# Kernel optimization log

Hardware: AMD Instinct MI355X
Metric: run time of the kernel (lower is better)

## Reference

```python
import jax, jax.numpy as jnp
import numpy as np

B, D, DK, DV, NH = 4, 256, 32, 32, 8
HS, WS, RATIO = 64, 64, 2
NQ = HS * WS
EPS_LN = 1e-5
EPS_IN = 1e-5


def setup_inputs() -> dict:
    key = jax.random.key(0)
    ks = jax.random.split(key, 16)
    f = jax.random.normal
    inp = {
        'query': f(ks[0], (B, NQ, D), jnp.float32),
        'key':   f(ks[1], (B, NQ, D), jnp.float32),
        'value': f(ks[2], (B, NQ, D), jnp.float32),
        # Linear weights stored (in, out); torch init std=0.001, bias 0 -- use small std for stability
        'Wq': f(ks[3], (D, DK * NH), jnp.float32) * 0.02,
        'bq': jnp.zeros((DK * NH,), jnp.float32),
        'Wk': f(ks[4], (D, DK * NH), jnp.float32) * 0.02,
        'bk': jnp.zeros((DK * NH,), jnp.float32),
        'Wv': f(ks[5], (D, DV * NH), jnp.float32) * 0.02,
        'bv': jnp.zeros((DV * NH,), jnp.float32),
        'Wo': f(ks[6], (NH * DV, D), jnp.float32) * 0.02,
        'bo': jnp.zeros((D,), jnp.float32),
        # sr_conv: Conv2d(D, D, k=ratio+1=3, stride=2, pad=1), OIHW
        'sr_w': f(ks[7], (D, D, 3, 3), jnp.float32) * (1.0 / np.sqrt(9 * D)),
        'sr_b': jnp.zeros((D,), jnp.float32),
        'ln_g': jnp.ones((D,), jnp.float32),
        'ln_b': jnp.zeros((D,), jnp.float32),
        # transform conv: Conv2d(h, h, 1) -> store as (h, h)
        'tf_w': f(ks[8], (NH, NH), jnp.float32) * (1.0 / np.sqrt(NH)),
        'tf_b': jnp.zeros((NH,), jnp.float32),
    }
    return inp


def _layernorm(x, g, b):
    mu = jnp.mean(x, axis=-1, keepdims=True)
    var = jnp.var(x, axis=-1, keepdims=True)
    return (x - mu) * jax.lax.rsqrt(var + EPS_LN) * g + b


def reference(query, key, value, Wq, bq, Wk, bk, Wv, bv, Wo, bo,
              sr_w, sr_b, ln_g, ln_b, tf_w, tf_b):
    b_s = query.shape[0]
    # q: (b, h, nq, dk)
    q = (query @ Wq + bq).reshape(b_s, NQ, NH, DK).transpose(0, 2, 1, 3)
    # spatial reduction of query: (b, c, H, W) -> conv stride 2 -> (b, c, H/2, W/2)
    x = query.transpose(0, 2, 1).reshape(b_s, D, HS, WS)
    x = jax.lax.conv_general_dilated(
        x, sr_w, window_strides=(RATIO, RATIO), padding=[(1, 1), (1, 1)],
        dimension_numbers=('NCHW', 'OIHW', 'NCHW')) + sr_b[None, :, None, None]
    nk = x.shape[2] * x.shape[3]
    x = x.reshape(b_s, D, nk).transpose(0, 2, 1)  # (b, nk, c)
    x = _layernorm(x, ln_g, ln_b)
    k = (x @ Wk + bk).reshape(b_s, nk, NH, DK).transpose(0, 2, 3, 1)  # (b,h,dk,nk)
    v = (x @ Wv + bv).reshape(b_s, nk, NH, DV).transpose(0, 2, 1, 3)  # (b,h,nk,dv)
    # scores (b,h,nq,nk)
    att = jnp.einsum('bhqd,bhdk->bhqk', q, k) / np.float32(np.sqrt(DK))
    # transform: 1x1 conv mixing heads, softmax over keys, InstanceNorm2d(h) (no affine)
    att = jnp.einsum('oi,biqk->boqk', tf_w, att) + tf_b[None, :, None, None]
    att = jax.nn.softmax(att, axis=-1)
    mu = jnp.mean(att, axis=(2, 3), keepdims=True)
    var = jnp.var(att, axis=(2, 3), keepdims=True)
    att = (att - mu) * jax.lax.rsqrt(var + EPS_IN)
    out = jnp.einsum('bhqk,bhkd->bhqd', att, v)  # (b,h,nq,dv)
    out = out.transpose(0, 2, 1, 3).reshape(b_s, NQ, NH * DV)
    return out @ Wo + bo
```

## Files before the change

kernel.cpp:

```cpp
#include <hip/hip_runtime.h>
#include <hip/hip_bf16.h>
#include <cstdint>


typedef _Float16 f16;
typedef f16 f16x4 __attribute__((ext_vector_type(4)));
typedef f16 f16x8 __attribute__((ext_vector_type(8)));
typedef float f32x4 __attribute__((ext_vector_type(4)));

__global__ void zero32_kernel(float* __restrict__ p){ p[threadIdx.x] = 0.f; }

__launch_bounds__(256)
__global__ void qcvt_kernel(const float* __restrict__ in, f16* __restrict__ out){
    size_t idx = ((size_t)blockIdx.x*256 + threadIdx.x) * 8;
    float4 a = *(const float4*)&in[idx];
    float4 b = *(const float4*)&in[idx+4];
    f16x8 h = { (f16)a.x,(f16)a.y,(f16)a.z,(f16)a.w,(f16)b.x,(f16)b.y,(f16)b.z,(f16)b.w };
    *(f16x8*)&out[idx] = h;
}

__launch_bounds__(256)
__global__ void wcvtT_kernel(const float* __restrict__ W, f16* __restrict__ WT){
    __shared__ float L[32][33];
    int r0 = blockIdx.x*32, c0 = blockIdx.y*32;
    int t = threadIdx.x;
    int rr = t >> 3, cc0 = (t & 7)*4;
    float4 v = *(const float4*)&W[(size_t)(r0+rr)*256 + c0 + cc0];
    L[rr][cc0] = v.x; L[rr][cc0+1] = v.y; L[rr][cc0+2] = v.z; L[rr][cc0+3] = v.w;
    __syncthreads();
    int c = t >> 3, rg = (t & 7)*4;
    f16x4 h = { (f16)L[rg][c], (f16)L[rg+1][c], (f16)L[rg+2][c], (f16)L[rg+3][c] };
    *(f16x4*)&WT[(size_t)(c0+c)*256 + r0 + rg] = h;
}

__launch_bounds__(256)
__global__ void convwT_kernel(const float* __restrict__ w, f16* __restrict__ wtT){
    int o = blockIdx.x, t = threadIdx.x;
    #pragma unroll
    for (int kk = 0; kk < 9; ++kk)
        wtT[(size_t)o*2304 + kk*256 + t] = (f16)w[(size_t)o*2304 + t*9 + kk];
}

template<int BM, int BN, bool OUTF16>
__launch_bounds__(256)
__global__ void mfma_gemm(const f16* __restrict__ A, const f16* __restrict__ BT,
                          const float* __restrict__ bias, void* __restrict__ Cout, int K){
    constexpr int MI = BM/32, NI = BN/32;
    __shared__ f16 As[BM][40];
    __shared__ f16 Bs[BN][40];
    int t = threadIdx.x;
    int wid = t >> 6, l = t & 63;
    int wr = wid >> 1, wc = wid & 1;
    int lr = l & 15, lg = l >> 4;
    int m0 = blockIdx.x * BM, n0 = blockIdx.y * BN;

    f32x4 acc[MI][NI] = {};
    for (int k0 = 0; k0 < K; k0 += 32){
        #pragma unroll
        for (int i = 0; i < BM/64; ++i){
            int e = t + i*256, r = e >> 2, c8 = (e & 3)*8;
            *(f16x8*)&As[r][c8] = *(const f16x8*)&A[(size_t)(m0+r)*K + k0 + c8];
        }
        #pragma unroll
        for (int i = 0; i < BN/64; ++i){
            int e = t + i*256, r = e >> 2, c8 = (e & 3)*8;
            *(f16x8*)&Bs[r][c8] = *(const f16x8*)&BT[(size_t)(n0+r)*K + k0 + c8];
        }
        __syncthreads();
        f16x8 af[MI], bf[NI];
        #pragma unroll
        for (int mi = 0; mi < MI; ++mi)
            af[mi] = *(const f16x8*)&As[wr*(BM/2) + mi*16 + lr][lg*8];
        #pragma unroll
        for (int ni = 0; ni < NI; ++ni)
            bf[ni] = *(const f16x8*)&Bs[wc*(BN/2) + ni*16 + lr][lg*8];
        #pragma unroll
        for (int mi = 0; mi < MI; ++mi)
            #pragma unroll
            for (int ni = 0; ni < NI; ++ni)
                acc[mi][ni] = __builtin_amdgcn_mfma_f32_16x16x32_f16(af[mi], bf[ni], acc[mi][ni], 0, 0, 0);
        __syncthreads();
    }
    #pragma unroll
    for (int mi = 0; mi < MI; ++mi){
        #pragma unroll
        for (int ni = 0; ni < NI; ++ni){
            int n = n0 + wc*(BN/2) + ni*16 + lr;
            float bv = bias[n];
            #pragma unroll
            for (int j = 0; j < 4; ++j){
                int m = m0 + wr*(BM/2) + mi*16 + lg*4 + j;
                float v = acc[mi][ni][j] + bv;
                if (OUTF16) ((f16*)Cout)[(size_t)m*256 + n] = (f16)v;
                else        ((float*)Cout)[(size_t)m*256 + n] = v;
            }
        }
    }
}

__launch_bounds__(256)
__global__ void conv_mfma_kernel(const f16* __restrict__ qh, const f16* __restrict__ wtT,
                                 const float* __restrict__ srb, float* __restrict__ Xc){
    __shared__ f16 As[64][40];
    __shared__ f16 Bs[64][40];
    int t = threadIdx.x;
    int wid = t >> 6, l = t & 63;
    int wr = wid >> 1, wc = wid & 1;
    int lr = l & 15, lg = l >> 4;
    int m0 = blockIdx.x * 64, n0 = blockIdx.y * 64;

    int r = t >> 2, c8 = (t & 3)*8;
    int m = m0 + r;
    int bb = m >> 10, pos = m & 1023;
    int oh = pos >> 5, ow = pos & 31;
    const f16* qb = qh + (size_t)bb*4096*256;

    f32x4 acc[2][2] = {};
    for (int k0 = 0; k0 < 2304; k0 += 32){
        int khkw = k0 >> 8;
        int kh = (khkw < 3) ? 0 : ((khkw < 6) ? 1 : 2);
        int kw = khkw - kh*3;
        int ih = oh*2 - 1 + kh, iw = ow*2 - 1 + kw;
        int kc = (k0 & 255) + c8;
        f16x8 av = {};
        if ((unsigned)ih < 64u && (unsigned)iw < 64u)
            av = *(const f16x8*)&qb[((size_t)(ih*64 + iw))*256 + kc];
        *(f16x8*)&As[r][c8] = av;
        *(f16x8*)&Bs[r][c8] = *(const f16x8*)&wtT[(size_t)(n0+r)*2304 + k0 + c8];
        __syncthreads();
        f16x8 af[2], bf[2];
        #pragma unroll
        for (int mi = 0; mi < 2; ++mi)
            af[mi] = *(const f16x8*)&As[wr*32 + mi*16 + lr][lg*8];
        #pragma unroll
        for (int ni = 0; ni < 2; ++ni)
            bf[ni] = *(const f16x8*)&Bs[wc*32 + ni*16 + lr][lg*8];
        #pragma unroll
        for (int mi = 0; mi < 2; ++mi)
            #pragma unroll
            for (int ni = 0; ni < 2; ++ni)
                acc[mi][ni] = __builtin_amdgcn_mfma_f32_16x16x32_f16(af[mi], bf[ni], acc[mi][ni], 0, 0, 0);
        __syncthreads();
    }
    #pragma unroll
    for (int mi = 0; mi < 2; ++mi){
        #pragma unroll
        for (int ni = 0; ni < 2; ++ni){
            int n = n0 + wc*32 + ni*16 + lr;
            float bv = srb[n];
            #pragma unroll
            for (int j = 0; j < 4; ++j){
                int mm = m0 + wr*32 + mi*16 + lg*4 + j;
                Xc[(size_t)mm*256 + n] = acc[mi][ni][j] + bv;
            }
        }
    }
}

__launch_bounds__(256)
__global__ void ln_kernel(const float* __restrict__ X, f16* __restrict__ Xo,
                          const float* __restrict__ g, const float* __restrict__ b){
    __shared__ float red[256];
    int row = blockIdx.x, t = threadIdx.x;
    float v = X[(size_t)row*256 + t];
    red[t] = v; __syncthreads();
    #pragma unroll
    for (int s=128; s>0; s>>=1){
        if (t < s) red[t] += red[t+s];
        __syncthreads();
    }
    float mu = red[0] * (1.f/256.f);
    __syncthreads();
    float dv = v - mu;
    red[t] = dv*dv; __syncthreads();
    #pragma unroll
    for (int s=128; s>0; s>>=1){
        if (t < s) red[t] += red[t+s];
        __syncthreads();
    }
    float var = red[0] * (1.f/256.f);
    Xo[(size_t)row*256 + t] = (f16)(dv * rsqrtf(var + 1e-5f) * g[t] + b[t]);
}

__launch_bounds__(256)
__global__ void vtran_kernel(const float* __restrict__ V, f16* __restrict__ VT){
    __shared__ float LT[32][33];
    int b = blockIdx.z, k0 = blockIdx.x*32, d0 = blockIdx.y*32;
    int t = threadIdx.x;
    int k = t >> 3, c0 = (t & 7)*4;
    float4 v = *(const float4*)&V[((size_t)(b*1024 + k0 + k))*256 + d0 + c0];
    LT[k][c0] = v.x; LT[k][c0+1] = v.y; LT[k][c0+2] = v.z; LT[k][c0+3] = v.w;
    __syncthreads();
    int d = t >> 3, kc0 = (t & 7)*4;
    f16x4 h = { (f16)LT[kc0][d], (f16)LT[kc0+1][d], (f16)LT[kc0+2][d], (f16)LT[kc0+3][d] };
    *(f16x4*)&VT[((size_t)(b*256 + d0 + d))*1024 + k0 + kc0] = h;
}

__launch_bounds__(256)
__global__ void colsum2_kernel(const f16* __restrict__ VT, float* __restrict__ csum){
    __shared__ float red[256];
    int bd = blockIdx.x, t = threadIdx.x;
    f16x4 h = *(const f16x4*)&VT[(size_t)bd*1024 + t*4];
    red[t] = (float)h[0] + (float)h[1] + (float)h[2] + (float)h[3];
    __syncthreads();
    #pragma unroll
    for (int s = 128; s > 0; s >>= 1){
        if (t < s) red[t] += red[t+s];
        __syncthreads();
    }
    if (t == 0) csum[bd] = red[0];
}

__launch_bounds__(512, 4)
__global__ void attn2_kernel(const f16* __restrict__ Qph, const f16* __restrict__ Kh,
                             const f16* __restrict__ VTh, const float* __restrict__ tfw,
                             const float* __restrict__ tfb, const float* __restrict__ csum,
                             float* __restrict__ outu, float* __restrict__ ssq){
    __shared__ f16 QL[32][264];
    __shared__ f16 KL[32][264];
    __shared__ f16 VTL[256][40];

    const int t  = threadIdx.x;
    const int bb = blockIdx.x >> 7;
    const int q0 = (blockIdx.x & 127) * 32;
    const int o  = t >> 6;
    const int l  = t & 63;
    const int g  = l >> 4;
    const int r  = l & 15;

    #pragma unroll
    for (int it = 0; it < 2; ++it){
        int e = t + it*512;
        int row = e >> 5, c0 = (e & 31)*8;
        *(f16x8*)&QL[row][c0] = *(const f16x8*)&Qph[((size_t)(bb*4096 + q0 + row))*256 + c0];
    }
    __syncthreads();

    const float tb = tfb[o];
    f16x8 qf[2][8];
    #pragma unroll
    for (int i = 0; i < 8; ++i){
        f16 sc = (f16)(tfw[o*8 + i] * 0.17677669529663687f);
        f16x8 scv = { sc,sc,sc,sc,sc,sc,sc,sc };
        #pragma unroll
        for (int qs = 0; qs < 2; ++qs){
            f16x8 v = *(const f16x8*)&QL[qs*16 + r][i*32 + g*8];
            qf[qs][i] = v * scv;
        }
    }

    f32x4 oacc[2][2] = { { {0,0,0,0},{0,0,0,0} }, { {0,0,0,0},{0,0,0,0} } };
    float s_part[2]  = {0.f, 0.f};
    float q2_part[2] = {0.f, 0.f};

    const f16* Khb = Kh  + (size_t)bb*1024*256;
    const f16* Vtb = VTh + (size_t)bb*256*1024;

    for (int kc = 0; kc < 1024; kc += 32){
        #pragma unroll
        for (int it = 0; it < 2; ++it){
            int e = t + it*512;
            int row = e >> 5, c = (e & 31)*8;
            *(f16x8*)&KL[row][c] = *(const f16x8*)&Khb[(size_t)(kc + row)*256 + c];
            int d = e >> 2, qt = (e & 3)*8;
            *(f16x8*)&VTL[d][qt] = *(const f16x8*)&Vtb[(size_t)d*1024 + kc + qt];
        }
        __syncthreads();
        #pragma unroll
        for (int ks = 0; ks < 2; ++ks){
            f16x8 kf[8];
            #pragma unroll
            for (int i = 0; i < 8; ++i)
                kf[i] = *(const f16x8*)&KL[ks*16 + r][i*32 + g*8];
            f16x4 va[2];
            #pragma unroll
            for (int dh = 0; dh < 2; ++dh)
                va[dh] = *(const f16x4*)&VTL[o*32 + dh*16 + r][ks*16 + g*4];
            #pragma unroll
            for (int qs = 0; qs < 2; ++qs){
                f32x4 acc = {0,0,0,0};
                #pragma unroll
                for (int i = 0; i < 8; ++i)
                    acc = __builtin_amdgcn_mfma_f32_16x16x32_f16(kf[i], qf[qs][i], acc, 0, 0, 0);
                f16x4 pb;
                float ps = 0.f, ps2 = 0.f;
                #pragma unroll
                for (int j = 0; j < 4; ++j){
                    float p = __expf(acc[j] + tb);
                    ps += p; ps2 += p*p;
                    pb[j] = (f16)(p - 1.0f);
                }
                s_part[qs]  += ps;
                q2_part[qs] += ps2;
                #pragma unroll
                for (int dh = 0; dh < 2; ++dh)
                    oacc[qs][dh] = __builtin_amdgcn_mfma_f32_16x16x16f16(va[dh], pb, oacc[qs][dh], 0, 0, 0);
            }
        }
        __syncthreads();
    }

    float s2tot = 0.f;
    #pragma unroll
    for (int qs = 0; qs < 2; ++qs){
        float s = s_part[qs];
        s += __shfl_xor(s, 16);
        s += __shfl_xor(s, 32);
        float inv = 1.0f / s;
        float corrf = (1.0f - s * (1.0f/1024.0f)) * inv;
        float q2 = q2_part[qs];
        q2 += __shfl_xor(q2, 16);
        q2 += __shfl_xor(q2, 32);
        s2tot += q2 * inv * inv;
        int q = q0 + qs*16 + r;
        #pragma unroll
        for (int dh = 0; dh < 2; ++dh){
            int d = o*32 + dh*16 + g*4;
            float4 cs = *(const float4*)&csum[bb*256 + d];
            float4 ov;
            ov.x = oacc[qs][dh][0]*inv + cs.x*corrf;
            ov.y = oacc[qs][dh][1]*inv + cs.y*corrf;
            ov.z = oacc[qs][dh][2]*inv + cs.z*corrf;
            ov.w = oacc[qs][dh][3]*inv + cs.w*corrf;
            *(float4*)&outu[((size_t)(bb*4096 + q))*256 + d] = ov;
        }
    }
    s2tot *= 0.25f;
    #pragma unroll
    for (int off = 1; off < 64; off <<= 1)
        s2tot += __shfl_xor(s2tot, off);
    if (l == 0) atomicAdd(&ssq[bb*8 + o], s2tot);
}

__global__ void rs_kernel(const float* __restrict__ ssq, float* __restrict__ rs){
    int t = threadIdx.x;
    const float mu = 1.f/1024.f;
    float var = ssq[t] * (1.f/(4096.f*1024.f)) - mu*mu;
    rs[t] = rsqrtf(var + 1e-5f);
}

__launch_bounds__(256)
__global__ void final_mfma_kernel(const float* __restrict__ A, const f16* __restrict__ WoT,
                                  const float* __restrict__ rsb, const float* __restrict__ bo,
                                  float* __restrict__ C){
    __shared__ f16 As[128][40];
    __shared__ f16 Bs[128][40];
    int t = threadIdx.x;
    int wid = t >> 6, l = t & 63;
    int wr = wid >> 1, wc = wid & 1;
    int lr = l & 15, lg = l >> 4;
    int m0 = blockIdx.x * 128, n0 = blockIdx.y * 128;
    int bbatch = m0 >> 12;

    f32x4 acc[4][4] = {};
    for (int k0 = 0; k0 < 256; k0 += 32){
        float rsk = rsb[bbatch*8 + (k0 >> 5)];
        #pragma unroll
        for (int i = 0; i < 2; ++i){
            int e = t + i*256, r = e >> 2, c8 = (e & 3)*8;
            const float* ap = &A[(size_t)(m0+r)*256 + k0 + c8];
            float4 v0 = *(const float4*)ap;
            float4 v1 = *(const float4*)(ap+4);
            f16x8 h = { (f16)(v0.x*rsk),(f16)(v0.y*rsk),(f16)(v0.z*rsk),(f16)(v0.w*rsk),
                        (f16)(v1.x*rsk),(f16)(v1.y*rsk),(f16)(v1.z*rsk),(f16)(v1.w*rsk) };
            *(f16x8*)&As[r][c8] = h;
        }
        #pragma unroll
        for (int i = 0; i < 2; ++i){
            int e = t + i*256, r = e >> 2, c8 = (e & 3)*8;
            *(f16x8*)&Bs[r][c8] = *(const f16x8*)&WoT[(size_t)(n0+r)*256 + k0 + c8];
        }
        __syncthreads();
        f16x8 af[4], bf[4];
        #pragma unroll
        for (int mi = 0; mi < 4; ++mi)
            af[mi] = *(const f16x8*)&As[wr*64 + mi*16 + lr][lg*8];
        #pragma unroll
        for (int ni = 0; ni < 4; ++ni)
            bf[ni] = *(const f16x8*)&Bs[wc*64 + ni*16 + lr][lg*8];
        #pragma unroll
        for (int mi = 0; mi < 4; ++mi)
            #pragma unroll
            for (int ni = 0; ni < 4; ++ni)
                acc[mi][ni] = __builtin_amdgcn_mfma_f32_16x16x32_f16(af[mi], bf[ni], acc[mi][ni], 0, 0, 0);
        __syncthreads();
    }
    #pragma unroll
    for (int mi = 0; mi < 4; ++mi){
        #pragma unroll
        for (int ni = 0; ni < 4; ++ni){
            int n = n0 + wc*64 + ni*16 + lr;
            float bv = bo[n];
            #pragma unroll
            for (int j = 0; j < 4; ++j){
                int m = m0 + wr*64 + mi*16 + lg*4 + j;
                C[(size_t)m*256 + n] = acc[mi][ni][j] + bv;
            }
        }
    }
}

extern "C" void kernel_launch(void* const* d_in, const int* in_sizes, int n_in,
                              void* d_out, int out_size, void* d_ws, size_t ws_size,
                              hipStream_t stream) {
    const float* query = (const float*)d_in[0];
    const float* Wq  = (const float*)d_in[3];
    const float* bq  = (const float*)d_in[4];
    const float* Wk  = (const float*)d_in[5];
    const float* bk  = (const float*)d_in[6];
    const float* Wv  = (const float*)d_in[7];
    const float* bv  = (const float*)d_in[8];
    const float* Wo  = (const float*)d_in[9];
    const float* bo  = (const float*)d_in[10];
    const float* srw = (const float*)d_in[11];
    const float* srb = (const float*)d_in[12];
    const float* lng = (const float*)d_in[13];
    const float* lnb = (const float*)d_in[14];
    const float* tfw = (const float*)d_in[15];
    const float* tfb = (const float*)d_in[16];
    float* out = (float*)d_out;

    float* ws = (float*)d_ws;
    float* outu  = ws;
    f16*   qh    = (f16*)(ws + 4194304);
    f16*   qbh   = (f16*)(ws + 6291456);
    float* xconv = ws + 8388608;
    float* vbuf  = ws + 9437184;
    f16*   xh    = (f16*)(ws + 10485760);
    f16*   kh    = (f16*)(ws + 11010048);
    f16*   vth   = (f16*)(ws + 11534336);
    f16*   wtT   = (f16*)(ws + 12058624);
    f16*   WqT   = (f16*)(ws + 12353536);
    f16*   WkT   = (f16*)(ws + 12386304);
    f16*   WvT   = (f16*)(ws + 12419072);
    f16*   WoT   = (f16*)(ws + 12451840);
    float* csum  = ws + 12484608;
    float* ssq   = ws + 12485632;
    float* rsb   = ws + 12485664;

    zero32_kernel<<<1, 32, 0, stream>>>(ssq);
    qcvt_kernel<<<2048, 256, 0, stream>>>(query, qh);
    wcvtT_kernel<<<dim3(8,8), 256, 0, stream>>>(Wq, WqT);
    wcvtT_kernel<<<dim3(8,8), 256, 0, stream>>>(Wk, WkT);
    wcvtT_kernel<<<dim3(8,8), 256, 0, stream>>>(Wv, WvT);
    wcvtT_kernel<<<dim3(8,8), 256, 0, stream>>>(Wo, WoT);
    convwT_kernel<<<256, 256, 0, stream>>>(srw, wtT);

    mfma_gemm<128,128,true><<<dim3(128,2), 256, 0, stream>>>(qh, WqT, bq, qbh, 256);
    conv_mfma_kernel<<<dim3(64,4), 256, 0, stream>>>(qh, wtT, srb, xconv);
    ln_kernel<<<4096, 256, 0, stream>>>(xconv, xh, lng, lnb);
    mfma_gemm<64,64,true><<<dim3(64,4), 256, 0, stream>>>(xh, WkT, bk, kh, 256);
    mfma_gemm<64,64,false><<<dim3(64,4), 256, 0, stream>>>(xh, WvT, bv, vbuf, 256);
    vtran_kernel<<<dim3(32, 8, 4), 256, 0, stream>>>(vbuf, vth);
    colsum2_kernel<<<1024, 256, 0, stream>>>(vth, csum);
    attn2_kernel<<<512, 512, 0, stream>>>(qbh, kh, vth, tfw, tfb, csum, outu, ssq);
    rs_kernel<<<1, 32, 0, stream>>>(ssq, rsb);
    final_mfma_kernel<<<dim3(128,2), 256, 0, stream>>>(outu, WoT, rsb, bo, out);
}
```

Baseline: 323.9 us.

## Double-buffer GEMM/conv/attention tiles and fuse V transpose, colsum, and zeroing

Adds register-prefetched double-buffered LDS staging to the projection GEMMs, the strided conv, the attention loop and the output GEMM, cutting one barrier per K-step and overlapping global loads with MFMA. The V projection now writes the transposed fp16 V directly and accumulates column sums with atomics, which removes the vtran and colsum kernels and the fp32 V buffer. Zeroing is folded into the query conversion, the four weight transposes are batched into one launch, and the attention softmax uses exp2 with log2e folded into the scale. This costs more shared memory per block, which may lower occupancy, and the atomic column sums make the summation order nondeterministic.

```diff
diff --git a/kernel.cpp b/kernel.cpp
--- a/kernel.cpp
+++ b/kernel.cpp
@@ -8,19 +8,28 @@
 typedef f16 f16x8 __attribute__((ext_vector_type(8)));
 typedef float f32x4 __attribute__((ext_vector_type(4)));
 
-__global__ void zero32_kernel(float* __restrict__ p){ p[threadIdx.x] = 0.f; }
-
-__launch_bounds__(256)
-__global__ void qcvt_kernel(const float* __restrict__ in, f16* __restrict__ out){
+__launch_bounds__(256)
+__global__ void qcvt_zero_kernel(const float* __restrict__ in, f16* __restrict__ out,
+                                 float* __restrict__ csum, float* __restrict__ ssq){
     size_t idx = ((size_t)blockIdx.x*256 + threadIdx.x) * 8;
     float4 a = *(const float4*)&in[idx];
     float4 b = *(const float4*)&in[idx+4];
     f16x8 h = { (f16)a.x,(f16)a.y,(f16)a.z,(f16)a.w,(f16)b.x,(f16)b.y,(f16)b.z,(f16)b.w };
     *(f16x8*)&out[idx] = h;
-}
-
-__launch_bounds__(256)
-__global__ void wcvtT_kernel(const float* __restrict__ W, f16* __restrict__ WT){
+    if (blockIdx.x == 0){
+        #pragma unroll
+        for (int i = 0; i < 4; ++i) csum[threadIdx.x + i*256] = 0.f;
+        if (threadIdx.x < 32) ssq[threadIdx.x] = 0.f;
+    }
+}
+
+__launch_bounds__(256)
+__global__ void wcvtT4_kernel(const float* __restrict__ W0, const float* __restrict__ W1,
+                              const float* __restrict__ W2, const float* __restrict__ W3,
+                              f16* __restrict__ T0, f16* __restrict__ T1,
+                              f16* __restrict__ T2, f16* __restrict__ T3){
+    const float* W = (blockIdx.z==0)?W0:(blockIdx.z==1)?W1:(blockIdx.z==2)?W2:W3;
+    f16* WT = (blockIdx.z==0)?T0:(blockIdx.z==1)?T1:(blockIdx.z==2)?T2:T3;
     __shared__ float L[32][33];
     int r0 = blockIdx.x*32, c0 = blockIdx.y*32;
     int t = threadIdx.x;
@@ -41,106 +50,161 @@
         wtT[(size_t)o*2304 + kk*256 + t] = (f16)w[(size_t)o*2304 + t*9 + kk];
 }
 
-template<int BM, int BN, bool OUTF16>
-__launch_bounds__(256)
-__global__ void mfma_gemm(const f16* __restrict__ A, const f16* __restrict__ BT,
-                          const float* __restrict__ bias, void* __restrict__ Cout, int K){
+template<int BM, int BN, int OUTMODE>
+__launch_bounds__(256)
+__global__ void mfma_gemm2(const f16* __restrict__ A, const f16* __restrict__ BT,
+                           const float* __restrict__ bias, void* __restrict__ Cout,
+                           f16* __restrict__ VT, float* __restrict__ csum, int K){
     constexpr int MI = BM/32, NI = BN/32;
-    __shared__ f16 As[BM][40];
-    __shared__ f16 Bs[BN][40];
+    constexpr int AL = BM/64, BL = BN/64;
+    __shared__ f16 As[2][BM][40];
+    __shared__ f16 Bs[2][BN][40];
     int t = threadIdx.x;
     int wid = t >> 6, l = t & 63;
     int wr = wid >> 1, wc = wid & 1;
     int lr = l & 15, lg = l >> 4;
     int m0 = blockIdx.x * BM, n0 = blockIdx.y * BN;
+    int r = t >> 2, c8 = (t & 3)*8;
+
+    f16x8 ra[AL], rb[BL];
+    auto loadc = [&](int k0){
+        #pragma unroll
+        for (int i = 0; i < AL; ++i)
+            ra[i] = *(const f16x8*)&A[(size_t)(m0 + r + i*64)*K + k0 + c8];
+        #pragma unroll
+        for (int i = 0; i < BL; ++i)
+            rb[i] = *(const f16x8*)&BT[(size_t)(n0 + r + i*64)*K + k0 + c8];
+    };
+    auto writec = [&](int b){
+        #pragma unroll
+        for (int i = 0; i < AL; ++i) *(f16x8*)&As[b][r + i*64][c8] = ra[i];
+        #pragma unroll
+        for (int i = 0; i < BL; ++i) *(f16x8*)&Bs[b][r + i*64][c8] = rb[i];
+    };
+
+    loadc(0); writec(0); loadc(32);
+    __syncthreads();
 
     f32x4 acc[MI][NI] = {};
-    for (int k0 = 0; k0 < K; k0 += 32){
-        #pragma unroll
-        for (int i = 0; i < BM/64; ++i){
-            int e = t + i*256, r = e >> 2, c8 = (e & 3)*8;
-            *(f16x8*)&As[r][c8] = *(const f16x8*)&A[(size_t)(m0+r)*K + k0 + c8];
-        }
-        #pragma unroll
-        for (int i = 0; i < BN/64; ++i){
-            int e = t + i*256, r = e >> 2, c8 = (e & 3)*8;
-            *(f16x8*)&Bs[r][c8] = *(const f16x8*)&BT[(size_t)(n0+r)*K + k0 + c8];
-        }
-        __syncthreads();
+    const int nsteps = K >> 5;
+    for (int s = 0; s < nsteps; ++s){
+        int cb = s & 1;
         f16x8 af[MI], bf[NI];
         #pragma unroll
         for (int mi = 0; mi < MI; ++mi)
-            af[mi] = *(const f16x8*)&As[wr*(BM/2) + mi*16 + lr][lg*8];
+            af[mi] = *(const f16x8*)&As[cb][wr*(BM/2) + mi*16 + lr][lg*8];
         #pragma unroll
         for (int ni = 0; ni < NI; ++ni)
-            bf[ni] = *(const f16x8*)&Bs[wc*(BN/2) + ni*16 + lr][lg*8];
+            bf[ni] = *(const f16x8*)&Bs[cb][wc*(BN/2) + ni*16 + lr][lg*8];
+        if (s + 1 < nsteps){
+            writec(cb^1);
+            if (s + 2 < nsteps) loadc((s+2)*32);
+        }
         #pragma unroll
         for (int mi = 0; mi < MI; ++mi)
             #pragma unroll
             for (int ni = 0; ni < NI; ++ni)
                 acc[mi][ni] = __builtin_amdgcn_mfma_f32_16x16x32_f16(af[mi], bf[ni], acc[mi][ni], 0, 0, 0);
-        __syncthreads();
-    }
-    #pragma unroll
-    for (int mi = 0; mi < MI; ++mi){
+        if (s + 1 < nsteps) __syncthreads();
+    }
+
+    if (OUTMODE == 1){
+        #pragma unroll
+        for (int mi = 0; mi < MI; ++mi){
+            #pragma unroll
+            for (int ni = 0; ni < NI; ++ni){
+                int n = n0 + wc*(BN/2) + ni*16 + lr;
+                float bv = bias[n];
+                #pragma unroll
+                for (int j = 0; j < 4; ++j){
+                    int m = m0 + wr*(BM/2) + mi*16 + lg*4 + j;
+                    ((f16*)Cout)[(size_t)m*256 + n] = (f16)(acc[mi][ni][j] + bv);
+                }
+            }
+        }
+    } else {
+        int b = m0 >> 10;
         #pragma unroll
         for (int ni = 0; ni < NI; ++ni){
             int n = n0 + wc*(BN/2) + ni*16 + lr;
             float bv = bias[n];
-            #pragma unroll
-            for (int j = 0; j < 4; ++j){
-                int m = m0 + wr*(BM/2) + mi*16 + lg*4 + j;
-                float v = acc[mi][ni][j] + bv;
-                if (OUTF16) ((f16*)Cout)[(size_t)m*256 + n] = (f16)v;
-                else        ((float*)Cout)[(size_t)m*256 + n] = v;
-            }
-        }
-    }
-}
-
-__launch_bounds__(256)
-__global__ void conv_mfma_kernel(const f16* __restrict__ qh, const f16* __restrict__ wtT,
-                                 const float* __restrict__ srb, float* __restrict__ Xc){
-    __shared__ f16 As[64][40];
-    __shared__ f16 Bs[64][40];
+            float csp = 0.f;
+            #pragma unroll
+            for (int mi = 0; mi < MI; ++mi){
+                f16x4 hv;
+                #pragma unroll
+                for (int j = 0; j < 4; ++j){
+                    f16 h = (f16)(acc[mi][ni][j] + bv);
+                    hv[j] = h;
+                    csp += (float)h;
+                }
+                int m = m0 + wr*(BM/2) + mi*16 + lg*4;
+                *(f16x4*)&VT[((size_t)(b*256 + n))*1024 + (m & 1023)] = hv;
+            }
+            csp += __shfl_xor(csp, 16);
+            csp += __shfl_xor(csp, 32);
+            if (lg == 0) atomicAdd(&csum[b*256 + n], csp);
+        }
+    }
+}
+
+__launch_bounds__(256)
+__global__ void conv2_kernel(const f16* __restrict__ qh, const f16* __restrict__ wtT,
+                             const float* __restrict__ srb, float* __restrict__ Xc){
+    __shared__ f16 As[2][64][40];
+    __shared__ f16 Bs[2][64][40];
     int t = threadIdx.x;
     int wid = t >> 6, l = t & 63;
     int wr = wid >> 1, wc = wid & 1;
     int lr = l & 15, lg = l >> 4;
     int m0 = blockIdx.x * 64, n0 = blockIdx.y * 64;
-
     int r = t >> 2, c8 = (t & 3)*8;
     int m = m0 + r;
-    int bb = m >> 10, pos = m & 1023;
+    int bbq = m >> 10, pos = m & 1023;
     int oh = pos >> 5, ow = pos & 31;
-    const f16* qb = qh + (size_t)bb*4096*256;
-
-    f32x4 acc[2][2] = {};
-    for (int k0 = 0; k0 < 2304; k0 += 32){
+    const f16* qb = qh + (size_t)bbq*4096*256;
+
+    f16x8 ra, rbv;
+    auto loadc = [&](int k0){
         int khkw = k0 >> 8;
         int kh = (khkw < 3) ? 0 : ((khkw < 6) ? 1 : 2);
         int kw = khkw - kh*3;
         int ih = oh*2 - 1 + kh, iw = ow*2 - 1 + kw;
         int kc = (k0 & 255) + c8;
-        f16x8 av = {};
+        f16x8 v = {};
         if ((unsigned)ih < 64u && (unsigned)iw < 64u)
-            av = *(const f16x8*)&qb[((size_t)(ih*64 + iw))*256 + kc];
-        *(f16x8*)&As[r][c8] = av;
-        *(f16x8*)&Bs[r][c8] = *(const f16x8*)&wtT[(size_t)(n0+r)*2304 + k0 + c8];
-        __syncthreads();
+            v = *(const f16x8*)&qb[((size_t)(ih*64 + iw))*256 + kc];
+        ra = v;
+        rbv = *(const f16x8*)&wtT[(size_t)(n0+r)*2304 + k0 + c8];
+    };
+    auto writec = [&](int b){
+        *(f16x8*)&As[b][r][c8] = ra;
+        *(f16x8*)&Bs[b][r][c8] = rbv;
+    };
+
+    loadc(0); writec(0); loadc(32);
+    __syncthreads();
+
+    f32x4 acc[2][2] = {};
+    for (int s = 0; s < 72; ++s){
+        int cb = s & 1;
         f16x8 af[2], bf[2];
         #pragma unroll
         for (int mi = 0; mi < 2; ++mi)
-            af[mi] = *(const f16x8*)&As[wr*32 + mi*16 + lr][lg*8];
+            af[mi] = *(const f16x8*)&As[cb][wr*32 + mi*16 + lr][lg*8];
         #pragma unroll
         for (int ni = 0; ni < 2; ++ni)
-            bf[ni] = *(const f16x8*)&Bs[wc*32 + ni*16 + lr][lg*8];
+            bf[ni] = *(const f16x8*)&Bs[cb][wc*32 + ni*16 + lr][lg*8];
+        if (s < 71){
+            writec(cb^1);
+            if (s < 70) loadc((s+2)*32);
+        }
         #pragma unroll
         for (int mi = 0; mi < 2; ++mi)
             #pragma unroll
             for (int ni = 0; ni < 2; ++ni)
                 acc[mi][ni] = __builtin_amdgcn_mfma_f32_16x16x32_f16(af[mi], bf[ni], acc[mi][ni], 0, 0, 0);
-        __syncthreads();
+        if (s < 71) __syncthreads();
     }
     #pragma unroll
     for (int mi = 0; mi < 2; ++mi){
@@ -182,43 +246,14 @@
     Xo[(size_t)row*256 + t] = (f16)(dv * rsqrtf(var + 1e-5f) * g[t] + b[t]);
 }
 
-__launch_bounds__(256)
-__global__ void vtran_kernel(const float* __restrict__ V, f16* __restrict__ VT){
-    __shared__ float LT[32][33];
-    int b = blockIdx.z, k0 = blockIdx.x*32, d0 = blockIdx.y*32;
-    int t = threadIdx.x;
-    int k = t >> 3, c0 = (t & 7)*4;
-    float4 v = *(const float4*)&V[((size_t)(b*1024 + k0 + k))*256 + d0 + c0];
-    LT[k][c0] = v.x; LT[k][c0+1] = v.y; LT[k][c0+2] = v.z; LT[k][c0+3] = v.w;
-    __syncthreads();
-    int d = t >> 3, kc0 = (t & 7)*4;
-    f16x4 h = { (f16)LT[kc0][d], (f16)LT[kc0+1][d], (f16)LT[kc0+2][d], (f16)LT[kc0+3][d] };
-    *(f16x4*)&VT[((size_t)(b*256 + d0 + d))*1024 + k0 + kc0] = h;
-}
-
-__launch_bounds__(256)
-__global__ void colsum2_kernel(const f16* __restrict__ VT, float* __restrict__ csum){
-    __shared__ float red[256];
-    int bd = blockIdx.x, t = threadIdx.x;
-    f16x4 h = *(const f16x4*)&VT[(size_t)bd*1024 + t*4];
-    red[t] = (float)h[0] + (float)h[1] + (float)h[2] + (float)h[3];
-    __syncthreads();
-    #pragma unroll
-    for (int s = 128; s > 0; s >>= 1){
-        if (t < s) red[t] += red[t+s];
-        __syncthreads();
-    }
-    if (t == 0) csum[bd] = red[0];
-}
-
 __launch_bounds__(512, 4)
-__global__ void attn2_kernel(const f16* __restrict__ Qph, const f16* __restrict__ Kh,
+__global__ void attn3_kernel(const f16* __restrict__ Qph, const f16* __restrict__ Kh,
                              const f16* __restrict__ VTh, const float* __restrict__ tfw,
                              const float* __restrict__ tfb, const float* __restrict__ csum,
                              float* __restrict__ outu, float* __restrict__ ssq){
-    __shared__ f16 QL[32][264];
-    __shared__ f16 KL[32][264];
-    __shared__ f16 VTL[256][40];
+    __shared__ f16 KL[2][32][264];
+    __shared__ f16 VTL[2][256][40];
+    f16 (*QL)[264] = KL[1];
 
     const int t  = threadIdx.x;
     const int bb = blockIdx.x >> 7;
@@ -228,19 +263,49 @@
     const int g  = l >> 4;
     const int r  = l & 15;
 
+    const f16* Khb = Kh  + (size_t)bb*1024*256;
+    const f16* Vtb = VTh + (size_t)bb*256*1024;
+
+    f16x8 rk[2], rv[2];
     #pragma unroll
     for (int it = 0; it < 2; ++it){
         int e = t + it*512;
-        int row = e >> 5, c0 = (e & 31)*8;
-        *(f16x8*)&QL[row][c0] = *(const f16x8*)&Qph[((size_t)(bb*4096 + q0 + row))*256 + c0];
-    }
-    __syncthreads();
-
-    const float tb = tfb[o];
+        int row = e >> 5, c = (e & 31)*8;
+        rk[it] = *(const f16x8*)&Khb[(size_t)row*256 + c];
+        int d = e >> 2, qt = (e & 3)*8;
+        rv[it] = *(const f16x8*)&Vtb[(size_t)d*1024 + qt];
+    }
+    #pragma unroll
+    for (int it = 0; it < 2; ++it){
+        int e = t + it*512;
+        int row = e >> 5, c = (e & 31)*8;
+        f16x8 qv = *(const f16x8*)&Qph[((size_t)(bb*4096 + q0 + row))*256 + c];
+        *(f16x8*)&QL[row][c] = qv;
+    }
+    #pragma unroll
+    for (int it = 0; it < 2; ++it){
+        int e = t + it*512;
+        int row = e >> 5, c = (e & 31)*8;
+        *(f16x8*)&KL[0][row][c] = rk[it];
+        int d = e >> 2, qt = (e & 3)*8;
+        *(f16x8*)&VTL[0][d][qt] = rv[it];
+    }
+    #pragma unroll
+    for (int it = 0; it < 2; ++it){
+        int e = t + it*512;
+        int row = e >> 5, c = (e & 31)*8;
+        rk[it] = *(const f16x8*)&Khb[(size_t)(32 + row)*256 + c];
+        int d = e >> 2, qt = (e & 3)*8;
+        rv[it] = *(const f16x8*)&Vtb[(size_t)d*1024 + 32 + qt];
+    }
+    __syncthreads();
+
+    const float LOG2E = 1.4426950408889634f;
+    const float tb2 = tfb[o] * LOG2E;
     f16x8 qf[2][8];
     #pragma unroll
     for (int i = 0; i < 8; ++i){
-        f16 sc = (f16)(tfw[o*8 + i] * 0.17677669529663687f);
+        f16 sc = (f16)(tfw[o*8 + i] * (0.17677669529663687f * LOG2E));
         f16x8 scv = { sc,sc,sc,sc,sc,sc,sc,sc };
         #pragma unroll
         for (int qs = 0; qs < 2; ++qs){
@@ -248,56 +313,67 @@
             qf[qs][i] = v * scv;
         }
     }
+    __syncthreads();
 
     f32x4 oacc[2][2] = { { {0,0,0,0},{0,0,0,0} }, { {0,0,0,0},{0,0,0,0} } };
     float s_part[2]  = {0.f, 0.f};
     float q2_part[2] = {0.f, 0.f};
 
-    const f16* Khb = Kh  + (size_t)bb*1024*256;
-    const f16* Vtb = VTh + (size_t)bb*256*1024;
-
-    for (int kc = 0; kc < 1024; kc += 32){
-        #pragma unroll
-        for (int it = 0; it < 2; ++it){
-            int e = t + it*512;
-            int row = e >> 5, c = (e & 31)*8;
-            *(f16x8*)&KL[row][c] = *(const f16x8*)&Khb[(size_t)(kc + row)*256 + c];
-            int d = e >> 2, qt = (e & 3)*8;
-            *(f16x8*)&VTL[d][qt] = *(const f16x8*)&Vtb[(size_t)d*1024 + kc + qt];
-        }
-        __syncthreads();
+    for (int kci = 0; kci < 32; ++kci){
+        const int cb = kci & 1;
+        const f16 (*KLc)[264] = KL[cb];
+        const f16 (*VTLc)[40] = VTL[cb];
+
         #pragma unroll
         for (int ks = 0; ks < 2; ++ks){
-            f16x8 kf[8];
-            #pragma unroll
-            for (int i = 0; i < 8; ++i)
-                kf[i] = *(const f16x8*)&KL[ks*16 + r][i*32 + g*8];
-            f16x4 va[2];
-            #pragma unroll
-            for (int dh = 0; dh < 2; ++dh)
-                va[dh] = *(const f16x4*)&VTL[o*32 + dh*16 + r][ks*16 + g*4];
+            f16x4 va0 = *(const f16x4*)&VTLc[o*32 + r][ks*16 + g*4];
+            f16x4 va1 = *(const f16x4*)&VTLc[o*32 + 16 + r][ks*16 + g*4];
+            f32x4 a0 = {0,0,0,0}, a1 = {0,0,0,0};
+            #pragma unroll
+            for (int i = 0; i < 8; ++i){
+                f16x8 kk = *(const f16x8*)&KLc[ks*16 + r][i*32 + g*8];
+                a0 = __builtin_amdgcn_mfma_f32_16x16x32_f16(kk, qf[0][i], a0, 0, 0, 0);
+                a1 = __builtin_amdgcn_mfma_f32_16x16x32_f16(kk, qf[1][i], a1, 0, 0, 0);
+            }
             #pragma unroll
             for (int qs = 0; qs < 2; ++qs){
-                f32x4 acc = {0,0,0,0};
-                #pragma unroll
-                for (int i = 0; i < 8; ++i)
-                    acc = __builtin_amdgcn_mfma_f32_16x16x32_f16(kf[i], qf[qs][i], acc, 0, 0, 0);
+                f32x4 aa = qs ? a1 : a0;
                 f16x4 pb;
                 float ps = 0.f, ps2 = 0.f;
                 #pragma unroll
                 for (int j = 0; j < 4; ++j){
-                    float p = __expf(acc[j] + tb);
+                    float p = exp2f(aa[j] + tb2);
                     ps += p; ps2 += p*p;
                     pb[j] = (f16)(p - 1.0f);
                 }
                 s_part[qs]  += ps;
                 q2_part[qs] += ps2;
+                oacc[qs][0] = __builtin_amdgcn_mfma_f32_16x16x16f16(va0, pb, oacc[qs][0], 0, 0, 0);
+                oacc[qs][1] = __builtin_amdgcn_mfma_f32_16x16x16f16(va1, pb, oacc[qs][1], 0, 0, 0);
+            }
+            if (ks == 0 && kci < 31){
                 #pragma unroll
-                for (int dh = 0; dh < 2; ++dh)
-                    oacc[qs][dh] = __builtin_amdgcn_mfma_f32_16x16x16f16(va[dh], pb, oacc[qs][dh], 0, 0, 0);
-            }
-        }
-        __syncthreads();
+                for (int it = 0; it < 2; ++it){
+                    int e = t + it*512;
+                    int row = e >> 5, c = (e & 31)*8;
+                    *(f16x8*)&KL[cb^1][row][c] = rk[it];
+                    int d = e >> 2, qt = (e & 3)*8;
+                    *(f16x8*)&VTL[cb^1][d][qt] = rv[it];
+                }
+                if (kci < 30){
+                    int kc2 = (kci + 2) * 32;
+                    #pragma unroll
+                    for (int it = 0; it < 2; ++it){
+                        int e = t + it*512;
+                        int row = e >> 5, c = (e & 31)*8;
+                        rk[it] = *(const f16x8*)&Khb[(size_t)(kc2 + row)*256 + c];
+                        int d = e >> 2, qt = (e & 3)*8;
+                        rv[it] = *(const f16x8*)&Vtb[(size_t)d*1024 + kc2 + qt];
+                    }
+                }
+            }
+        }
+        if (kci < 31) __syncthreads();
     }
 
     float s2tot = 0.f;
@@ -340,50 +416,69 @@
 }
 
 __launch_bounds__(256)
-__global__ void final_mfma_kernel(const float* __restrict__ A, const f16* __restrict__ WoT,
-                                  const float* __restrict__ rsb, const float* __restrict__ bo,
-                                  float* __restrict__ C){
-    __shared__ f16 As[128][40];
-    __shared__ f16 Bs[128][40];
+__global__ void final2_kernel(const float* __restrict__ A, const f16* __restrict__ WoT,
+                              const float* __restrict__ rsb, const float* __restrict__ bo,
+                              float* __restrict__ C){
+    __shared__ f16 As[2][128][40];
+    __shared__ f16 Bs[2][128][40];
     int t = threadIdx.x;
     int wid = t >> 6, l = t & 63;
     int wr = wid >> 1, wc = wid & 1;
     int lr = l & 15, lg = l >> 4;
     int m0 = blockIdx.x * 128, n0 = blockIdx.y * 128;
     int bbatch = m0 >> 12;
-
-    f32x4 acc[4][4] = {};
-    for (int k0 = 0; k0 < 256; k0 += 32){
-        float rsk = rsb[bbatch*8 + (k0 >> 5)];
+    int r = t >> 2, c8 = (t & 3)*8;
+
+    float rs8[8];
+    #pragma unroll
+    for (int i = 0; i < 8; ++i) rs8[i] = rsb[bbatch*8 + i];
+
+    float4 rfa[4];
+    f16x8 rbv[2];
+    auto loadc = [&](int k0){
         #pragma unroll
         for (int i = 0; i < 2; ++i){
-            int e = t + i*256, r = e >> 2, c8 = (e & 3)*8;
-            const float* ap = &A[(size_t)(m0+r)*256 + k0 + c8];
-            float4 v0 = *(const float4*)ap;
-            float4 v1 = *(const float4*)(ap+4);
+            const float* ap = &A[(size_t)(m0 + r + i*64)*256 + k0 + c8];
+            rfa[2*i]   = *(const float4*)ap;
+            rfa[2*i+1] = *(const float4*)(ap+4);
+            rbv[i] = *(const f16x8*)&WoT[(size_t)(n0 + r + i*64)*256 + k0 + c8];
+        }
+    };
+    auto writec = [&](int b, int k0){
+        float rsk = rs8[k0 >> 5];
+        #pragma unroll
+        for (int i = 0; i < 2; ++i){
+            float4 v0 = rfa[2*i], v1 = rfa[2*i+1];
             f16x8 h = { (f16)(v0.x*rsk),(f16)(v0.y*rsk),(f16)(v0.z*rsk),(f16)(v0.w*rsk),
                         (f16)(v1.x*rsk),(f16)(v1.y*rsk),(f16)(v1.z*rsk),(f16)(v1.w*rsk) };
-            *(f16x8*)&As[r][c8] = h;
-        }
-        #pragma unroll
-        for (int i = 0; i < 2; ++i){
-            int e = t + i*256, r = e >> 2, c8 = (e & 3)*8;
-            *(f16x8*)&Bs[r][c8] = *(const f16x8*)&WoT[(size_t)(n0+r)*256 + k0 + c8];
-        }
-        __syncthreads();
+            *(f16x8*)&As[b][r + i*64][c8] = h;
+            *(f16x8*)&Bs[b][r + i*64][c8] = rbv[i];
+        }
+    };
+
+    loadc(0); writec(0, 0); loadc(32);
+    __syncthreads();
+
+    f32x4 acc[4][4] = {};
+    for (int s = 0; s < 8; ++s){
+        int cb = s & 1;
         f16x8 af[4], bf[4];
         #pragma unroll
         for (int mi = 0; mi < 4; ++mi)
-            af[mi] = *(const f16x8*)&As[wr*64 + mi*16 + lr][lg*8];
+            af[mi] = *(const f16x8*)&As[cb][wr*64 + mi*16 + lr][lg*8];
         #pragma unroll
         for (int ni = 0; ni < 4; ++ni)
-            bf[ni] = *(const f16x8*)&Bs[wc*64 + ni*16 + lr][lg*8];
+            bf[ni] = *(const f16x8*)&Bs[cb][wc*64 + ni*16 + lr][lg*8];
+        if (s < 7){
+            writec(cb^1, (s+1)*32);
+            if (s < 6) loadc((s+2)*32);
+        }
         #pragma unroll
         for (int mi = 0; mi < 4; ++mi)
             #pragma unroll
             for (int ni = 0; ni < 4; ++ni)
                 acc[mi][ni] = __builtin_amdgcn_mfma_f32_16x16x32_f16(af[mi], bf[ni], acc[mi][ni], 0, 0, 0);
-        __syncthreads();
+        if (s < 7) __syncthreads();
     }
     #pragma unroll
     for (int mi = 0; mi < 4; ++mi){
@@ -425,35 +520,28 @@
     f16*   qh    = (f16*)(ws + 4194304);
     f16*   qbh   = (f16*)(ws + 6291456);
     float* xconv = ws + 8388608;
-    float* vbuf  = ws + 9437184;
-    f16*   xh    = (f16*)(ws + 10485760);
-    f16*   kh    = (f16*)(ws + 11010048);
-    f16*   vth   = (f16*)(ws + 11534336);
-    f16*   wtT   = (f16*)(ws + 12058624);
-    f16*   WqT   = (f16*)(ws + 12353536);
-    f16*   WkT   = (f16*)(ws + 12386304);
-    f16*   WvT   = (f16*)(ws + 12419072);
-    f16*   WoT   = (f16*)(ws + 12451840);
-    float* csum  = ws + 12484608;
-    float* ssq   = ws + 12485632;
-    float* rsb   = ws + 12485664;
-
-    zero32_kernel<<<1, 32, 0, stream>>>(ssq);
-    qcvt_kernel<<<2048, 256, 0, stream>>>(query, qh);
-    wcvtT_kernel<<<dim3(8,8), 256, 0, stream>>>(Wq, WqT);
-    wcvtT_kernel<<<dim3(8,8), 256, 0, stream>>>(Wk, WkT);
-    wcvtT_kernel<<<dim3(8,8), 256, 0, stream>>>(Wv, WvT);
-    wcvtT_kernel<<<dim3(8,8), 256, 0, stream>>>(Wo, WoT);
+    f16*   xh    = (f16*)(ws + 9437184);
+    f16*   kh    = (f16*)(ws + 9961472);
+    f16*   vth   = (f16*)(ws + 10485760);
+    f16*   wtT   = (f16*)(ws + 11010048);
+    f16*   WqT   = (f16*)(ws + 11304960);
+    f16*   WkT   = (f16*)(ws + 11337728);
+    f16*   WvT   = (f16*)(ws + 11370496);
+    f16*   WoT   = (f16*)(ws + 11403264);
+    float* csum  = ws + 11436032;
+    float* ssq   = ws + 11437056;
+    float* rsb   = ws + 11437088;
+
+    qcvt_zero_kernel<<<2048, 256, 0, stream>>>(query, qh, csum, ssq);
+    wcvtT4_kernel<<<dim3(8,8,4), 256, 0, stream>>>(Wq, Wk, Wv, Wo, WqT, WkT, WvT, WoT);
     convwT_kernel<<<256, 256, 0, stream>>>(srw, wtT);
 
-    mfma_gemm<128,128,true><<<dim3(128,2), 256, 0, stream>>>(qh, WqT, bq, qbh, 256);
-    conv_mfma_kernel<<<dim3(64,4), 256, 0, stream>>>(qh, wtT, srb, xconv);
+    mfma_gemm2<128,128,1><<<dim3(128,2), 256, 0, stream>>>(qh, WqT, bq, qbh, nullptr, nullptr, 256);
+    conv2_kernel<<<dim3(64,4), 256, 0, stream>>>(qh, wtT, srb, xconv);
     ln_kernel<<<4096, 256, 0, stream>>>(xconv, xh, lng, lnb);
-    mfma_gemm<64,64,true><<<dim3(64,4), 256, 0, stream>>>(xh, WkT, bk, kh, 256);
-    mfma_gemm<64,64,false><<<dim3(64,4), 256, 0, stream>>>(xh, WvT, bv, vbuf, 256);
-    vtran_kernel<<<dim3(32, 8, 4), 256, 0, stream>>>(vbuf, vth);
-    colsum2_kernel<<<1024, 256, 0, stream>>>(vth, csum);
-    attn2_kernel<<<512, 512, 0, stream>>>(qbh, kh, vth, tfw, tfb, csum, outu, ssq);
+    mfma_gemm2<64,64,1><<<dim3(64,4), 256, 0, stream>>>(xh, WkT, bk, kh, nullptr, nullptr, 256);
+    mfma_gemm2<64,64,2><<<dim3(64,4), 256, 0, stream>>>(xh, WvT, bv, nullptr, vth, csum, 256);
+    attn3_kernel<<<512, 512, 0, stream>>>(qbh, kh, vth, tfw, tfb, csum, outu, ssq);
     rs_kernel<<<1, 32, 0, stream>>>(ssq, rsb);
-    final_mfma_kernel<<<dim3(128,2), 256, 0, stream>>>(outu, WoT, rsb, bo, out);
-}
+    final2_kernel<<<dim3(128,2), 256, 0, stream>>>(outu, WoT, rsb, bo, out);
+}
```

After: 356.6 us. 10.1% more time.
